# Kernel optimization log

Measured on AMD Instinct MI355X. Metric: run time of the kernel, lower is better.

## Reference

```python
import jax, jax.numpy as jnp
import numpy as np

B, N, IN_DIM, HIDDEN, N_CLASS = 32768, 25, 3, 128, 2

# BODY_25 skeleton edges from the repo
_SRC = np.array([17, 15, 18, 16, 0, 2, 3, 4, 5, 6, 7, 8, 9, 12, 10, 13, 11, 14, 23, 22, 24, 20, 19, 21])
_DST = np.array([15, 0, 16, 0, 1, 1, 2, 3, 1, 5, 6, 1, 8, 8, 9, 12, 10, 13, 22, 11, 11, 19, 14, 14])


def setup_inputs() -> dict:
    key = jax.random.key(0)
    ks = jax.random.split(key, 4)
    # skeleton edges + self loops (dgl.add_self_loop)
    src = jnp.asarray(np.concatenate([_SRC, np.arange(N)]), dtype=jnp.int64)
    dst = jnp.asarray(np.concatenate([_DST, np.arange(N)]), dtype=jnp.int64)
    return {
        "x": jax.random.normal(ks[0], (B, N, IN_DIM), dtype=jnp.float32),
        "src": src,
        "dst": dst,
        "W1": jax.random.normal(ks[1], (IN_DIM, HIDDEN), dtype=jnp.float32) / np.sqrt(IN_DIM),
        "b1": jnp.zeros((HIDDEN,), jnp.float32),
        "W2": jax.random.normal(ks[2], (HIDDEN, HIDDEN), dtype=jnp.float32) / np.sqrt(HIDDEN),
        "b2": jnp.zeros((HIDDEN,), jnp.float32),
        "Wfc": jax.random.normal(ks[3], (HIDDEN, N_CLASS), dtype=jnp.float32) / np.sqrt(HIDDEN),
        "bfc": jnp.zeros((N_CLASS,), jnp.float32),
    }


def reference(x, src, dst, W1, b1, W2, b2, Wfc, bfc):
    # x: [B, N, F] node features for B identical-topology skeleton graphs
    Bn, Nn, _ = x.shape
    ones = jnp.ones(src.shape, x.dtype)
    deg_out = jax.ops.segment_sum(ones, src, num_segments=Nn)  # [N]
    deg_in = jax.ops.segment_sum(ones, dst, num_segments=Nn)   # [N]
    # DGL GraphConv norm='both': D_in^{-1/2} A D_out^{-1/2} X W + b
    cs = jnp.where(deg_out > 0, deg_out ** -0.5, 0.0)
    ci = jnp.where(deg_in > 0, deg_in ** -0.5, 0.0)

    def gconv(h, W, b):
        msg = h[:, src, :] * cs[src][None, :, None]            # gather + src norm
        agg = jnp.zeros_like(h).at[:, dst, :].add(msg)          # scatter-add
        agg = agg * ci[None, :, None]                           # dst norm
        return agg @ W + b

    h = jax.nn.relu(gconv(x, W1, b1))
    h = jax.nn.relu(gconv(h, W2, b2))
    pooled = jnp.mean(h, axis=1)  # dgl.mean_nodes -> [B, HIDDEN]
    return pooled @ Wfc + bfc      # [B, N_CLASS]
```

## Files before the change

### kernel.cpp

```cpp
#include <hip/hip_runtime.h>

#define NN    25
#define FIN   3
#define HID   128
#define GPB   4
#define STRDQ 68

typedef int i32x4 __attribute__((ext_vector_type(4)));
typedef unsigned int uint;

__global__ void w2_absmax(const float* __restrict__ W2, float* __restrict__ scales)
{
    __shared__ float red[256];
    int tid = threadIdx.x;
    float m = 1e-20f;
    for (int i = tid; i < HID * HID; i += 256) m = fmaxf(m, fabsf(W2[i]));
    red[tid] = m;
    __syncthreads();
    for (int s = 128; s > 0; s >>= 1) {
        if (tid < s) red[tid] = fmaxf(red[tid], red[tid + s]);
        __syncthreads();
    }
    if (tid == 0) { scales[0] = red[0]; scales[1] = 32000.0f / red[0]; }
}

static __device__ __forceinline__ long pack8(const int* q)
{
    unsigned long v = 0;
    #pragma unroll
    for (int j = 0; j < 8; ++j)
        v |= ((unsigned long)(unsigned char)(q[j] & 255)) << (8 * j);
    return (long)v;
}

__global__ void pack_w2_i8(const float* __restrict__ W2, const float* __restrict__ scales,
                           long* __restrict__ w2q)
{
    int gi = blockIdx.x * blockDim.x + threadIdx.x;
    if (gi >= 4096) return;
    int l  = gi & 63;
    int nt = (gi >> 6) & 7;
    int kt = (gi >> 9) & 3;
    int p  = gi >> 11;
    int n  = nt * 16 + (l & 15);
    int kb = kt * 32 + (l >> 4) * 8;
    float Sb = scales[1];
    int q8[8];
    #pragma unroll
    for (int j = 0; j < 8; ++j) {
        int qv = (int)rintf(W2[(kb + j) * HID + n] * Sb);
        qv = min(max(qv, -32600), 32600);
        int lo = ((qv + 128) & 255) - 128;
        int hi = (qv - lo) >> 8;
        q8[j] = p ? lo : hi;
    }
    w2q[gi] = pack8(q8);
}

static __device__ __forceinline__ void agg25_inplace(float2* A)
{
    const float cA = 0.40824829f;
    const float cB = 0.31622777f;
    const float cC = 0.44721360f;
    const float cH = 0.5f;
    const float cS = 0.70710678f;
    A[1]  = cB * (A[0] + A[2] + A[5] + A[8]) + cC * A[1];
    A[0]  = cA * (A[15] + A[16] + A[0]);
    A[2]  = cH * (A[3]  + A[2]);
    A[3]  = cH * (A[4]  + A[3]);
    A[4]  = cS *  A[4];
    A[5]  = cH * (A[6]  + A[5]);
    A[6]  = cH * (A[7]  + A[6]);
    A[7]  = cS *  A[7];
    A[8]  = cA * (A[9] + A[12] + A[8]);
    A[9]  = cH * (A[10] + A[9]);
    A[10] = cH * (A[11] + A[10]);
    A[11] = cA * (A[22] + A[24] + A[11]);
    A[12] = cH * (A[13] + A[12]);
    A[13] = cH * (A[14] + A[13]);
    A[14] = cA * (A[19] + A[21] + A[14]);
    A[15] = cH * (A[17] + A[15]);
    A[16] = cH * (A[18] + A[16]);
    A[17] = cS *  A[17];
    A[18] = cS *  A[18];
    A[19] = cH * (A[20] + A[19]);
    A[20] = cS *  A[20];
    A[21] = cS *  A[21];
    A[22] = cH * (A[23] + A[22]);
    A[23] = cS *  A[23];
    A[24] = cS *  A[24];
}

static __device__ __forceinline__ void unpack16(uint4 d, long& hi, long& lo)
{
    uint h01 = __builtin_amdgcn_perm(d.y, d.x, 0x07050301u) ^ 0x80808080u;
    uint h23 = __builtin_amdgcn_perm(d.w, d.z, 0x07050301u) ^ 0x80808080u;
    uint l01 = __builtin_amdgcn_perm(d.y, d.x, 0x06040200u) ^ 0x80808080u;
    uint l23 = __builtin_amdgcn_perm(d.w, d.z, 0x06040200u) ^ 0x80808080u;
    uint hv[2] = {h01, h23};
    uint lv[2] = {l01, l23};
    __builtin_memcpy(&hi, hv, 8);
    __builtin_memcpy(&lo, lv, 8);
}

__global__ __launch_bounds__(256, 5) void gcn_main(
    const float* __restrict__ x,
    const float* __restrict__ W1, const float* __restrict__ b1,
    const float* __restrict__ b2,
    const float* __restrict__ Wfc, const float* __restrict__ bfc,
    const long* __restrict__ w2q, const float* __restrict__ scales,
    float* __restrict__ out)
{
    __shared__ __align__(16) uint  bufQ[GPB][NN][STRDQ];
    __shared__ __align__(16) float xs[GPB][80];
    __shared__ float s_b2[HID];
    __shared__ float s_wfc[HID * 2];
    __shared__ float s_bfc[2];

    const int tid  = threadIdx.x;
    const int w    = tid >> 6;
    const int lane = tid & 63;
    const int g    = blockIdx.x * GPB + w;
    const int c0   = lane * 2;
    const int m0   = lane & 15;
    const int quad = lane >> 4;

    if (tid < HID) s_b2[tid] = b2[tid];
    s_wfc[tid] = Wfc[tid];
    if (tid < 2) s_bfc[tid] = bfc[tid];
    __syncthreads();

    const float Sb = scales[1];
    float msk1[4];
    #pragma unroll
    for (int rr = 0; rr < 4; ++rr)
        msk1[rr] = (quad * 4 + rr < 9) ? 1.0f : 0.0f;

    const float* xg = x + (size_t)g * (NN * FIN);
    xs[w][lane] = xg[lane];
    if (lane < NN * FIN - 64) xs[w][64 + lane] = xg[64 + lane];
    asm volatile("s_waitcnt lgkmcnt(0)" ::: "memory");

    float2 w1r0 = *(const float2*)(W1 + 0 * HID + c0);
    float2 w1r1 = *(const float2*)(W1 + 1 * HID + c0);
    float2 w1r2 = *(const float2*)(W1 + 2 * HID + c0);
    float2 A[NN];
    const float4* xv = (const float4*)&xs[w][0];
    #pragma unroll
    for (int grp = 0; grp < 6; ++grp) {
        float4 p = xv[grp * 3 + 0];
        float4 q = xv[grp * 3 + 1];
        float4 r = xv[grp * 3 + 2];
        float xa[4][3] = {{p.x, p.y, p.z}, {p.w, q.x, q.y},
                          {q.z, q.w, r.x}, {r.y, r.z, r.w}};
        #pragma unroll
        for (int j = 0; j < 4; ++j) {
            int n = grp * 4 + j;
            A[n].x = fmaf(xa[j][0], w1r0.x, fmaf(xa[j][1], w1r1.x, xa[j][2] * w1r2.x));
            A[n].y = fmaf(xa[j][0], w1r0.y, fmaf(xa[j][1], w1r1.y, xa[j][2] * w1r2.y));
        }
    }
    {
        float x0 = xs[w][72], x1 = xs[w][73], x2 = xs[w][74];
        A[24].x = fmaf(x0, w1r0.x, fmaf(x1, w1r1.x, x2 * w1r2.x));
        A[24].y = fmaf(x0, w1r0.y, fmaf(x1, w1r1.y, x2 * w1r2.y));
    }

    float2 b1v = *(const float2*)(b1 + c0);
    agg25_inplace(A);
    #pragma unroll
    for (int n = 0; n < NN; ++n) {
        A[n].x = fmaxf(A[n].x + b1v.x, 0.0f);
        A[n].y = fmaxf(A[n].y + b1v.y, 0.0f);
    }

    agg25_inplace(A);

    float am = 1e-20f;
    #pragma unroll
    for (int n = 0; n < NN; ++n)
        am = fmaxf(am, fmaxf(fabsf(A[n].x), fabsf(A[n].y)));
    #pragma unroll
    for (int off = 32; off > 0; off >>= 1)
        am = fmaxf(am, __shfl_xor(am, off));
    const float Sa = 32000.0f / am;

    #pragma unroll
    for (int n = 0; n < NN; ++n) {
        uint qx = (uint)fmaf(A[n].x, Sa, 32896.5f);
        uint qy = (uint)fmaf(A[n].y, Sa, 32896.5f);
        bufQ[w][n][lane] = __builtin_amdgcn_perm(qy, qx, 0x05040100u);
    }
    asm volatile("s_waitcnt lgkmcnt(0)" ::: "memory");

    const int m1  = min(16 + m0, NN - 1);
    const int kq4 = quad * 4;

    long ah[2][4], al[2][4];
    #pragma unroll
    for (int kt = 0; kt < 4; ++kt) {
        uint4 d0 = *(const uint4*)&bufQ[w][m0][kt * 16 + kq4];
        uint4 d1 = *(const uint4*)&bufQ[w][m1][kt * 16 + kq4];
        unpack16(d0, ah[0][kt], al[0][kt]);
        unpack16(d1, ah[1][kt], al[1][kt]);
    }

    const float rsL = 256.0f / (Sa * Sb);

    float s0 = 0.0f, s1 = 0.0f;
    #pragma unroll
    for (int nt = 0; nt < 8; ++nt) {
        i32x4 aHH[2], aX[2];
        #pragma unroll
        for (int mt = 0; mt < 2; ++mt) { aHH[mt] = (i32x4)0; aX[mt] = (i32x4)0; }

        #pragma unroll
        for (int kt = 0; kt < 4; ++kt) {
            long bh = w2q[(size_t)(((0 + kt) * 8 + nt) * 64 + lane)];
            long bl = w2q[(size_t)(((4 + kt) * 8 + nt) * 64 + lane)];
            aHH[0] = __builtin_amdgcn_mfma_i32_16x16x32_i8(ah[0][kt], bh, aHH[0], 0, 0, 0);
            aHH[1] = __builtin_amdgcn_mfma_i32_16x16x32_i8(ah[1][kt], bh, aHH[1], 0, 0, 0);
            aX[0]  = __builtin_amdgcn_mfma_i32_16x16x32_i8(ah[0][kt], bl, aX[0], 0, 0, 0);
            aX[0]  = __builtin_amdgcn_mfma_i32_16x16x32_i8(al[0][kt], bh, aX[0], 0, 0, 0);
            aX[1]  = __builtin_amdgcn_mfma_i32_16x16x32_i8(ah[1][kt], bl, aX[1], 0, 0, 0);
            aX[1]  = __builtin_amdgcn_mfma_i32_16x16x32_i8(al[1][kt], bh, aX[1], 0, 0, 0);
        }

        float b2c = s_b2[nt * 16 + m0];
        float2 wfc = *(const float2*)&s_wfc[(nt * 16 + m0) * 2];
        float s = 0.0f;
        #pragma unroll
        for (int rr = 0; rr < 4; ++rr) {
            int ci = (int)(((uint)aHH[0][rr] << 8)) + aX[0][rr];
            s += fmaxf(fmaf((float)ci, rsL, b2c), 0.0f);
        }
        #pragma unroll
        for (int rr = 0; rr < 4; ++rr) {
            int ci = (int)(((uint)aHH[1][rr] << 8)) + aX[1][rr];
            float hv = fmaxf(fmaf((float)ci, rsL, b2c), 0.0f);
            s = fmaf(hv, msk1[rr], s);
        }
        s0 = fmaf(s, wfc.x, s0);
        s1 = fmaf(s, wfc.y, s1);
    }

    #pragma unroll
    for (int off = 32; off > 0; off >>= 1) {
        s0 += __shfl_down(s0, off);
        s1 += __shfl_down(s1, off);
    }
    if (lane == 0) {
        out[g * 2 + 0] = s0 * (1.0f / 25.0f) + s_bfc[0];
        out[g * 2 + 1] = s1 * (1.0f / 25.0f) + s_bfc[1];
    }
}

extern "C" void kernel_launch(void* const* d_in, const int* in_sizes, int n_in,
                              void* d_out, int out_size, void* d_ws, size_t ws_size,
                              hipStream_t stream)
{
    const float* x   = (const float*)d_in[0];
    const float* W1  = (const float*)d_in[3];
    const float* b1  = (const float*)d_in[4];
    const float* W2  = (const float*)d_in[5];
    const float* b2  = (const float*)d_in[6];
    const float* Wfc = (const float*)d_in[7];
    const float* bfc = (const float*)d_in[8];
    float* out = (float*)d_out;

    const int Btot = in_sizes[0] / (NN * FIN);

    float* scales = (float*)d_ws;
    long*  w2q    = (long*)((char*)d_ws + 256);

    hipLaunchKernelGGL(w2_absmax, dim3(1), dim3(256), 0, stream, W2, scales);
    hipLaunchKernelGGL(pack_w2_i8, dim3(16), dim3(256), 0, stream, W2, scales, w2q);
    hipLaunchKernelGGL(gcn_main, dim3(Btot / GPB), dim3(256), 0, stream,
                       x, W1, b1, b2, Wfc, bfc, w2q, scales, out);
}
```

Baseline: 179.6 us.

## Shrink LDS with XOR-swizzled buffer, fold bias into int accumulator, drop block sync

Removes the shared-memory staging of b2/Wfc/bfc and the block-wide barrier, reusing the per-wave quantized buffer to hold x and packing it without padding using an XOR swizzle to avoid bank conflicts. The b2 bias is pre-quantized into the integer accumulator init, and the rescale is moved to the final output, so the epilogue becomes an integer max and convert. Launch bounds go from 5 to 6 blocks per CU to exploit the smaller LDS footprint. Bias rounding adds small quantization error, and the extra occupancy target may add register pressure or spills.

```diff
diff --git a/kernel.cpp b/kernel.cpp
--- a/kernel.cpp
+++ b/kernel.cpp
@@ -4,7 +4,7 @@
 #define FIN   3
 #define HID   128
 #define GPB   4
-#define STRDQ 68
+#define ROWDW 64
 
 typedef int i32x4 __attribute__((ext_vector_type(4)));
 typedef unsigned int uint;
@@ -103,7 +103,7 @@
     __builtin_memcpy(&lo, lv, 8);
 }
 
-__global__ __launch_bounds__(256, 5) void gcn_main(
+__global__ __launch_bounds__(256, 6) void gcn_main(
     const float* __restrict__ x,
     const float* __restrict__ W1, const float* __restrict__ b1,
     const float* __restrict__ b2,
@@ -111,11 +111,7 @@
     const long* __restrict__ w2q, const float* __restrict__ scales,
     float* __restrict__ out)
 {
-    __shared__ __align__(16) uint  bufQ[GPB][NN][STRDQ];
-    __shared__ __align__(16) float xs[GPB][80];
-    __shared__ float s_b2[HID];
-    __shared__ float s_wfc[HID * 2];
-    __shared__ float s_bfc[2];
+    __shared__ __align__(16) uint bufQ[GPB][NN * ROWDW];
 
     const int tid  = threadIdx.x;
     const int w    = tid >> 6;
@@ -125,27 +121,23 @@
     const int m0   = lane & 15;
     const int quad = lane >> 4;
 
-    if (tid < HID) s_b2[tid] = b2[tid];
-    s_wfc[tid] = Wfc[tid];
-    if (tid < 2) s_bfc[tid] = bfc[tid];
-    __syncthreads();
-
     const float Sb = scales[1];
     float msk1[4];
     #pragma unroll
     for (int rr = 0; rr < 4; ++rr)
         msk1[rr] = (quad * 4 + rr < 9) ? 1.0f : 0.0f;
 
+    float* xsw = (float*)bufQ[w];
     const float* xg = x + (size_t)g * (NN * FIN);
-    xs[w][lane] = xg[lane];
-    if (lane < NN * FIN - 64) xs[w][64 + lane] = xg[64 + lane];
+    xsw[lane] = xg[lane];
+    if (lane < NN * FIN - 64) xsw[64 + lane] = xg[64 + lane];
     asm volatile("s_waitcnt lgkmcnt(0)" ::: "memory");
 
     float2 w1r0 = *(const float2*)(W1 + 0 * HID + c0);
     float2 w1r1 = *(const float2*)(W1 + 1 * HID + c0);
     float2 w1r2 = *(const float2*)(W1 + 2 * HID + c0);
     float2 A[NN];
-    const float4* xv = (const float4*)&xs[w][0];
+    const float4* xv = (const float4*)bufQ[w];
     #pragma unroll
     for (int grp = 0; grp < 6; ++grp) {
         float4 p = xv[grp * 3 + 0];
@@ -161,7 +153,7 @@
         }
     }
     {
-        float x0 = xs[w][72], x1 = xs[w][73], x2 = xs[w][74];
+        float x0 = xsw[72], x1 = xsw[73], x2 = xsw[74];
         A[24].x = fmaf(x0, w1r0.x, fmaf(x1, w1r1.x, x2 * w1r2.x));
         A[24].y = fmaf(x0, w1r0.y, fmaf(x1, w1r1.y, x2 * w1r2.y));
     }
@@ -185,22 +177,32 @@
         am = fmaxf(am, __shfl_xor(am, off));
     const float Sa = 32000.0f / am;
 
+    const float invRs = Sa * Sb * (1.0f / 256.0f);
+    int b2q[8];
+    #pragma unroll
+    for (int t = 0; t < 8; ++t)
+        b2q[t] = (int)rintf(b2[t * 16 + m0] * invRs);
+
+    asm volatile("" ::: "memory");
+    const int blk = lane >> 2;
+    const int sub = lane & 3;
     #pragma unroll
     for (int n = 0; n < NN; ++n) {
         uint qx = (uint)fmaf(A[n].x, Sa, 32896.5f);
         uint qy = (uint)fmaf(A[n].y, Sa, 32896.5f);
-        bufQ[w][n][lane] = __builtin_amdgcn_perm(qy, qx, 0x05040100u);
+        int col = ((blk ^ (n & 15)) << 2) | sub;
+        bufQ[w][(n << 6) + col] = __builtin_amdgcn_perm(qy, qx, 0x05040100u);
     }
     asm volatile("s_waitcnt lgkmcnt(0)" ::: "memory");
 
-    const int m1  = min(16 + m0, NN - 1);
-    const int kq4 = quad * 4;
+    const int m1 = min(16 + m0, NN - 1);
 
     long ah[2][4], al[2][4];
     #pragma unroll
     for (int kt = 0; kt < 4; ++kt) {
-        uint4 d0 = *(const uint4*)&bufQ[w][m0][kt * 16 + kq4];
-        uint4 d1 = *(const uint4*)&bufQ[w][m1][kt * 16 + kq4];
+        int b = (kt << 2) | quad;
+        uint4 d0 = *(const uint4*)&bufQ[w][(m0 << 6) + ((b ^ m0) << 2)];
+        uint4 d1 = *(const uint4*)&bufQ[w][(m1 << 6) + ((b ^ (m1 & 15)) << 2)];
         unpack16(d0, ah[0][kt], al[0][kt]);
         unpack16(d1, ah[1][kt], al[1][kt]);
     }
@@ -210,9 +212,13 @@
     float s0 = 0.0f, s1 = 0.0f;
     #pragma unroll
     for (int nt = 0; nt < 8; ++nt) {
+        float2 wfc = *(const float2*)(Wfc + (nt * 16 + m0) * 2);
+
         i32x4 aHH[2], aX[2];
-        #pragma unroll
-        for (int mt = 0; mt < 2; ++mt) { aHH[mt] = (i32x4)0; aX[mt] = (i32x4)0; }
+        i32x4 bi;
+        bi[0] = b2q[nt]; bi[1] = b2q[nt]; bi[2] = b2q[nt]; bi[3] = b2q[nt];
+        aHH[0] = (i32x4)0; aHH[1] = (i32x4)0;
+        aX[0] = bi; aX[1] = bi;
 
         #pragma unroll
         for (int kt = 0; kt < 4; ++kt) {
@@ -226,19 +232,16 @@
             aX[1]  = __builtin_amdgcn_mfma_i32_16x16x32_i8(al[1][kt], bh, aX[1], 0, 0, 0);
         }
 
-        float b2c = s_b2[nt * 16 + m0];
-        float2 wfc = *(const float2*)&s_wfc[(nt * 16 + m0) * 2];
         float s = 0.0f;
         #pragma unroll
         for (int rr = 0; rr < 4; ++rr) {
             int ci = (int)(((uint)aHH[0][rr] << 8)) + aX[0][rr];
-            s += fmaxf(fmaf((float)ci, rsL, b2c), 0.0f);
+            s += (float)max(ci, 0);
         }
         #pragma unroll
         for (int rr = 0; rr < 4; ++rr) {
             int ci = (int)(((uint)aHH[1][rr] << 8)) + aX[1][rr];
-            float hv = fmaxf(fmaf((float)ci, rsL, b2c), 0.0f);
-            s = fmaf(hv, msk1[rr], s);
+            s = fmaf((float)max(ci, 0), msk1[rr], s);
         }
         s0 = fmaf(s, wfc.x, s0);
         s1 = fmaf(s, wfc.y, s1);
@@ -250,8 +253,9 @@
         s1 += __shfl_down(s1, off);
     }
     if (lane == 0) {
-        out[g * 2 + 0] = s0 * (1.0f / 25.0f) + s_bfc[0];
-        out[g * 2 + 1] = s1 * (1.0f / 25.0f) + s_bfc[1];
+        const float post = rsL * (1.0f / 25.0f);
+        out[g * 2 + 0] = fmaf(s0, post, bfc[0]);
+        out[g * 2 + 1] = fmaf(s1, post, bfc[1]);
     }
 }
 
```

Measured after the change: 437.5 us. 2.44x slower.
